# Optimization experiments

Hardware: AMD Instinct MI355X
Metric: run time of the kernel (lower is better)

Reference implementation:

```python
import jax, jax.numpy as jnp
import numpy as np
from jax import lax

SIGMA = 4
TOPK = 9
GRID = 28          # patch grid hardcoded in AnomalyMapGenerator
IMG = 224          # input_size
SCALE = IMG // GRID  # nearest-neighbor upsample factor = 8
KSIZE = 2 * int(4.0 * SIGMA + 0.5) + 1  # 33, as in compute_anomaly_map


def _gaussian_kernel1d():
    x = jnp.arange(KSIZE, dtype=jnp.float32) - KSIZE // 2
    g = jnp.exp(-(x * x) / (2.0 * SIGMA * SIGMA))
    return g / jnp.sum(g)


def _gaussian_blur2d(x):
    # x: [B,1,H,W]; separable gaussian with reflect padding (kornia default)
    g = _gaussian_kernel1d()
    pad = KSIZE // 2
    # blur along H
    xh = jnp.pad(x, ((0, 0), (0, 0), (pad, pad), (0, 0)), mode='reflect')
    xh = lax.conv_general_dilated(xh, g.reshape(1, 1, KSIZE, 1), (1, 1), 'VALID')
    # blur along W
    xw = jnp.pad(xh, ((0, 0), (0, 0), (0, 0), (pad, pad)), mode='reflect')
    return lax.conv_general_dilated(xw, g.reshape(1, 1, 1, KSIZE), (1, 1), 'VALID')


def setup_inputs() -> dict:
    key = jax.random.key(0)
    k1, k2 = jax.random.split(key)
    embedding = jax.random.normal(k1, (3136, 1536), dtype=jnp.float32)
    memory_bank = jax.random.normal(k2, (20000, 1536), dtype=jnp.float32)  # M x D
    return {"embedding": embedding, "memory_bank": memory_bank}


def reference(embedding, memory_bank):
    x2 = jnp.sum(embedding * embedding, axis=-1, keepdims=True)        # [N,1]
    y2 = jnp.sum(memory_bank * memory_bank, axis=-1)                   # [M]
    d2 = x2 + y2[None, :] - 2.0 * (embedding @ memory_bank.T)          # [N,M]
    dist = jnp.sqrt(jnp.maximum(d2, 0.0))
    # topk smallest, ascending (matches torch.topk largest=False)
    neg_top, _ = lax.top_k(-dist, TOPK)
    patch_scores = -neg_top                                            # [N,9]

    # --- compute_anomaly_map ---
    batch = patch_scores.shape[0] // (GRID * GRID)
    amap = patch_scores[:, 0].reshape(batch, 1, GRID, GRID)
    # F.interpolate default mode='nearest' with integer factor 8 == repeat
    amap = jnp.repeat(jnp.repeat(amap, SCALE, axis=2), SCALE, axis=3)  # [B,1,224,224]
    amap = _gaussian_blur2d(amap)

    # --- compute_anomaly_score ---
    idx = jnp.argmax(patch_scores[:, 0])
    confidence = patch_scores[idx]                                     # [9]
    e = jnp.exp(confidence)
    weights = 1.0 - jnp.max(e) / jnp.sum(e)
    score = weights * jnp.max(patch_scores[:, 0])
    return amap, score
```

## Files before the change

kernel.cpp:

```cpp
#include <hip/hip_runtime.h>

typedef __attribute__((ext_vector_type(4))) int i32x4;

#define N_ROWS 3136
#define M_COLS 20000
#define KDIM   1536
#define NCT    157
#define NRT    25
#define PPR    (NCT*9)

#define QSCL   (4.0f / 127.0f)
#define QINV   (127.0f / 4.0f)
#define TWO_S2 (2.0f * QSCL * QSCL)

#define GLOAD_LDS16(g, l) __builtin_amdgcn_global_load_lds( \
    (const __attribute__((address_space(1))) unsigned int*)(g), \
    (__attribute__((address_space(3))) unsigned int*)(l), 16, 0, 0)

__device__ inline void t9_insert(float (&t)[9], float v) {
    #pragma unroll
    for (int s = 8; s >= 1; --s)
        t[s] = __builtin_amdgcn_fmed3f(v, t[s-1], t[s]);
    t[0] = fminf(t[0], v);
}

__device__ inline int q8(float x) {
    int q = (int)rintf(x * QINV);
    q = q > 127 ? 127 : q;
    q = q < -127 ? -127 : q;
    return q & 255;
}

__global__ void cvt_norm_kernel(const float* __restrict__ src,
                                unsigned char* __restrict__ dst,
                                float* __restrict__ norms, int rows) {
    int lane = threadIdx.x & 63;
    int row = blockIdx.x * (blockDim.x >> 6) + (threadIdx.x >> 6);
    if (row >= rows) return;
    const float4* p = (const float4*)(src + (size_t)row * KDIM);
    int* q = (int*)(dst + (size_t)row * KDIM);
    float s = 0.f;
    #pragma unroll
    for (int i = 0; i < 6; ++i) {
        float4 v = p[lane + i * 64];
        s += v.x*v.x + v.y*v.y + v.z*v.z + v.w*v.w;
        q[lane + i * 64] = q8(v.x) | (q8(v.y) << 8) | (q8(v.z) << 16) | (q8(v.w) << 24);
    }
    #pragma unroll
    for (int off = 32; off > 0; off >>= 1) s += __shfl_down(s, off);
    if (lane == 0) norms[row] = s;
}

union SMem {
    unsigned char stg[2][16384];
    struct { float Ds[64 * 129]; float T9[3 * 64 * 9]; } epi;
};

#define STAGE(BUF, KT) do { \
    const int koff_ = (KT) * 64; \
    GLOAD_LDS16(pa[0] + koff_, sm.stg[BUF] + ldsoff[0]); \
    GLOAD_LDS16(pa[1] + koff_, sm.stg[BUF] + ldsoff[1]); \
    GLOAD_LDS16(pb[0] + koff_, sm.stg[BUF] + 8192 + ldsoff[0]); \
    GLOAD_LDS16(pb[1] + koff_, sm.stg[BUF] + 8192 + ldsoff[1]); \
} while (0)

#define KSTEP(CB, NB, KT, PF) do { \
    if (PF) STAGE(NB, (KT) + 1); \
    i32x4 af[4], bfr[4]; \
    _Pragma("unroll") \
    for (int mi = 0; mi < 4; ++mi) \
        af[mi] = *(const i32x4*)(sm.stg[CB] + (wr + mi * 16 + l15) * 64 + kbs); \
    _Pragma("unroll") \
    for (int ni = 0; ni < 4; ++ni) \
        bfr[ni] = *(const i32x4*)(sm.stg[CB] + 8192 + (wc + ni * 16 + l15) * 64 + kbs); \
    _Pragma("unroll") \
    for (int mi = 0; mi < 4; ++mi) \
        _Pragma("unroll") \
        for (int ni = 0; ni < 4; ++ni) \
            acc[mi][ni] = __builtin_amdgcn_mfma_i32_16x16x64_i8(af[mi], bfr[ni], acc[mi][ni], 0, 0, 0); \
    asm volatile("s_waitcnt vmcnt(0)" ::: "memory"); \
    __builtin_amdgcn_s_barrier(); \
} while (0)

__global__ __launch_bounds__(256, 4) void dist_topk_kernel(
    const unsigned char* __restrict__ Aq,
    const unsigned char* __restrict__ Bq,
    const float* __restrict__ x2, const float* __restrict__ y2,
    float* __restrict__ partials)
{
    __shared__ __align__(16) SMem sm;

    const int tid = threadIdx.x;
    const int ct = blockIdx.x, rt = blockIdx.y;
    const int rowBase = rt * 128, colBase = ct * 128;
    const int wave = tid >> 6, lane = tid & 63;

    const unsigned char* pa[2];
    const unsigned char* pb[2];
    int ldsoff[2];
    #pragma unroll
    for (int i = 0; i < 2; ++i) {
        int flat = i * 256 + tid;
        int r = flat >> 2;
        int kk = (((flat & 3) ^ ((flat >> 3) & 3))) * 16;
        int ar = rowBase + r; ar = ar < N_ROWS ? ar : N_ROWS - 1;
        int bc = colBase + r; bc = bc < M_COLS ? bc : M_COLS - 1;
        pa[i] = Aq + (size_t)ar * KDIM + kk;
        pb[i] = Bq + (size_t)bc * KDIM + kk;
        ldsoff[i] = flat * 16;
    }

    const int l15 = lane & 15;
    const int kb = (lane >> 4) * 16;
    const int kbs = kb ^ (((l15 >> 1) & 3) << 4);
    const int g4 = (lane >> 4) * 4;
    const int wr = (wave >> 1) * 64;
    const int wc = (wave & 1) * 64;

    i32x4 acc[4][4] = {};

    STAGE(0, 0);
    asm volatile("s_waitcnt vmcnt(0)" ::: "memory");
    __builtin_amdgcn_s_barrier();

    #pragma unroll 1
    for (int kt = 0; kt < 24; kt += 2) {
        KSTEP(0, 1, kt, 1);
        KSTEP(1, 0, kt + 1, (kt + 2) < 24);
    }

    int ncols = M_COLS - colBase; ncols = ncols < 128 ? ncols : 128;

    #pragma unroll
    for (int pass = 0; pass < 2; ++pass) {
        if ((wave >> 1) == pass) {
            #pragma unroll
            for (int ni = 0; ni < 4; ++ni) {
                int c = wc + ni * 16 + l15;
                int gc = colBase + c;
                float yv = y2[gc < M_COLS ? gc : M_COLS - 1];
                #pragma unroll
                for (int mi = 0; mi < 4; ++mi) {
                    #pragma unroll
                    for (int j = 0; j < 4; ++j) {
                        int rloc = mi * 16 + g4 + j;
                        int gr = rowBase + pass * 64 + rloc;
                        float xv = x2[gr < N_ROWS ? gr : N_ROWS - 1];
                        sm.epi.Ds[rloc * 129 + c] = xv + yv - TWO_S2 * (float)acc[mi][ni][j];
                    }
                }
            }
        }
        __syncthreads();
        int r = tid & 63, q = tid >> 6;
        int grow = rowBase + pass * 64 + r;
        float t9[9];
        #pragma unroll
        for (int s = 0; s < 9; ++s) t9[s] = 3.4e38f;
        int cs = q * 32;
        int ce = (cs + 32 < ncols) ? cs + 32 : ncols;
        for (int c = cs; c < ce; ++c) t9_insert(t9, sm.epi.Ds[r * 129 + c]);
        if (q > 0) {
            #pragma unroll
            for (int s = 0; s < 9; ++s) sm.epi.T9[((q - 1) * 64 + r) * 9 + s] = t9[s];
        }
        __syncthreads();
        if (q == 0 && grow < N_ROWS) {
            #pragma unroll
            for (int qq = 0; qq < 3; ++qq)
                #pragma unroll
                for (int s = 0; s < 9; ++s)
                    t9_insert(t9, sm.epi.T9[(qq * 64 + r) * 9 + s]);
            float* dst = partials + (size_t)grow * PPR + ct * 9;
            #pragma unroll
            for (int s = 0; s < 9; ++s) dst[s] = t9[s];
        }
        __syncthreads();
    }
}

__global__ void merge_topk_kernel(const float* __restrict__ partials,
                                  float* __restrict__ scores) {
    int lane = threadIdx.x & 63;
    int row = blockIdx.x * 4 + (threadIdx.x >> 6);
    const float* p = partials + (size_t)row * PPR;
    float t9[9];
    #pragma unroll
    for (int s = 0; s < 9; ++s) t9[s] = 3.4e38f;
    for (int i = lane; i < PPR; i += 64) {
        float v = p[i];
        if (v < t9[8]) t9_insert(t9, v);
    }
    #pragma unroll
    for (int off = 32; off > 0; off >>= 1) {
        float o[9];
        #pragma unroll
        for (int s = 0; s < 9; ++s) o[s] = __shfl_xor(t9[s], off);
        #pragma unroll
        for (int s = 0; s < 9; ++s)
            if (o[s] < t9[8]) t9_insert(t9, o[s]);
    }
    if (lane == 0) {
        #pragma unroll
        for (int s = 0; s < 9; ++s)
            scores[row * 9 + s] = sqrtf(fmaxf(t9[s], 0.f));
    }
}

__global__ void blur_h_kernel(const float* __restrict__ scores, float* __restrict__ tH) {
    int idx = blockIdx.x * blockDim.x + threadIdx.x;
    if (idx >= 4 * 224 * 28) return;
    int pw = idx % 28, y = (idx / 28) % 224, b = idx / (28 * 224);
    float acc = 0.f, gsum = 0.f;
    #pragma unroll
    for (int k = 0; k < 33; ++k) {
        float xk = (float)(k - 16);
        float w = expf(-xk * xk * (1.0f / 32.0f));
        gsum += w;
        int yy = y - 16 + k;
        yy = yy < 0 ? -yy : yy;
        yy = yy > 223 ? 446 - yy : yy;
        acc += w * scores[(size_t)(b * 784 + (yy >> 3) * 28 + pw) * 9];
    }
    tH[idx] = acc / gsum;
}

__global__ void blur_w_kernel(const float* __restrict__ tH, float* __restrict__ out) {
    int idx = blockIdx.x * blockDim.x + threadIdx.x;
    if (idx >= 4 * 224 * 224) return;
    int x = idx % 224, y = (idx / 224) % 224, b = idx / (224 * 224);
    float acc = 0.f, gsum = 0.f;
    #pragma unroll
    for (int k = 0; k < 33; ++k) {
        float xk = (float)(k - 16);
        float w = expf(-xk * xk * (1.0f / 32.0f));
        gsum += w;
        int xx = x - 16 + k;
        xx = xx < 0 ? -xx : xx;
        xx = xx > 223 ? 446 - xx : xx;
        acc += w * tH[(b * 224 + y) * 28 + (xx >> 3)];
    }
    out[idx] = acc / gsum;
}

__global__ void score_kernel(const float* __restrict__ scores, float* __restrict__ out) {
    __shared__ float vmax[256];
    __shared__ int   vidx[256];
    int tid = threadIdx.x;
    float best = -3.4e38f; int bi = 0x7fffffff;
    for (int r = tid; r < N_ROWS; r += 256) {
        float v = scores[r * 9];
        if (v > best) { best = v; bi = r; }
    }
    vmax[tid] = best; vidx[tid] = bi;
    __syncthreads();
    for (int s = 128; s > 0; s >>= 1) {
        if (tid < s) {
            if (vmax[tid + s] > vmax[tid] ||
                (vmax[tid + s] == vmax[tid] && vidx[tid + s] < vidx[tid])) {
                vmax[tid] = vmax[tid + s]; vidx[tid] = vidx[tid + s];
            }
        }
        __syncthreads();
    }
    if (tid == 0) {
        int idx = vidx[0];
        float es = 0.f, em = -3.4e38f;
        #pragma unroll
        for (int s = 0; s < 9; ++s) {
            float e = expf(scores[idx * 9 + s]);
            es += e; em = fmaxf(em, e);
        }
        out[4 * 224 * 224] = (1.0f - em / es) * vmax[0];
    }
}

extern "C" void kernel_launch(void* const* d_in, const int* in_sizes, int n_in,
                              void* d_out, int out_size, void* d_ws, size_t ws_size,
                              hipStream_t stream) {
    const float* emb = (const float*)d_in[0];
    const float* mb  = (const float*)d_in[1];
    float* out = (float*)d_out;
    char* ws = (char*)d_ws;

    unsigned char* mbq      = (unsigned char*)(ws);
    unsigned char* embq     = (unsigned char*)(ws + 30720000);
    float*         x2       = (float*)(ws + 35536896);
    float*         y2       = (float*)(ws + 35549440);
    float*         partials = (float*)(ws + 35629440);
    float*         scores   = (float*)(ws + 53354112);
    float*         tH       = (float*)(ws + 53467008);

    cvt_norm_kernel<<<M_COLS / 4, 256, 0, stream>>>(mb, mbq, y2, M_COLS);
    cvt_norm_kernel<<<N_ROWS / 4, 256, 0, stream>>>(emb, embq, x2, N_ROWS);
    dist_topk_kernel<<<dim3(NCT, NRT), 256, 0, stream>>>(embq, mbq, x2, y2, partials);
    merge_topk_kernel<<<N_ROWS / 4, 256, 0, stream>>>(partials, scores);
    blur_h_kernel<<<(4 * 224 * 28 + 255) / 256, 256, 0, stream>>>(scores, tH);
    blur_w_kernel<<<(4 * 224 * 224 + 255) / 256, 256, 0, stream>>>(tH, out);
    score_kernel<<<1, 256, 0, stream>>>(scores, out);
}
```

Baseline: 245.1 us.

## Remap workgroups per XCD and shrink epilogue LDS for higher occupancy

Launches the distance/top-k kernel as a 1D grid and remaps block IDs so consecutive tiles on each XCD share column tiles (ct-major order), which is meant to improve L2 reuse of memory-bank tiles. It also splits the epilogue into four 32-row passes using all 8 thread groups with a tree reduction, shrinking the Ds scratch and raising the launch-bounds occupancy hint from 4 to 5. The cost is more barriers and passes in the epilogue, and possibly more register pressure under the tighter bound.

```diff
diff --git a/kernel.cpp b/kernel.cpp
--- a/kernel.cpp
+++ b/kernel.cpp
@@ -7,6 +7,7 @@
 #define KDIM   1536
 #define NCT    157
 #define NRT    25
+#define NWG    (NCT * NRT)
 #define PPR    (NCT*9)
 
 #define QSCL   (4.0f / 127.0f)
@@ -53,7 +54,7 @@
 
 union SMem {
     unsigned char stg[2][16384];
-    struct { float Ds[64 * 129]; float T9[3 * 64 * 9]; } epi;
+    struct { float Ds[32 * 129]; float T9[8 * 32 * 9]; } epi;
 };
 
 #define STAGE(BUF, KT) do { \
@@ -82,7 +83,7 @@
     __builtin_amdgcn_s_barrier(); \
 } while (0)
 
-__global__ __launch_bounds__(256, 4) void dist_topk_kernel(
+__global__ __launch_bounds__(256, 5) void dist_topk_kernel(
     const unsigned char* __restrict__ Aq,
     const unsigned char* __restrict__ Bq,
     const float* __restrict__ x2, const float* __restrict__ y2,
@@ -91,9 +92,14 @@
     __shared__ __align__(16) SMem sm;
 
     const int tid = threadIdx.x;
-    const int ct = blockIdx.x, rt = blockIdx.y;
+    const int wave = tid >> 6, lane = tid & 63;
+
+    int orig = blockIdx.x;
+    int xcd = orig & 7, li = orig >> 3;
+    const int qc = NWG / 8, rc = NWG % 8;
+    int wg = (xcd < rc ? xcd * (qc + 1) : rc * (qc + 1) + (xcd - rc) * qc) + li;
+    const int ct = wg / NRT, rt = wg % NRT;
     const int rowBase = rt * 128, colBase = ct * 128;
-    const int wave = tid >> 6, lane = tid & 63;
 
     const unsigned char* pa[2];
     const unsigned char* pb[2];
@@ -132,50 +138,57 @@
     int ncols = M_COLS - colBase; ncols = ncols < 128 ? ncols : 128;
 
     #pragma unroll
-    for (int pass = 0; pass < 2; ++pass) {
-        if ((wave >> 1) == pass) {
+    for (int p = 0; p < 4; ++p) {
+        __syncthreads();
+        if ((wave >> 1) == (p >> 1)) {
+            const int mi0 = (p & 1) * 2;
             #pragma unroll
             for (int ni = 0; ni < 4; ++ni) {
                 int c = wc + ni * 16 + l15;
                 int gc = colBase + c;
                 float yv = y2[gc < M_COLS ? gc : M_COLS - 1];
                 #pragma unroll
-                for (int mi = 0; mi < 4; ++mi) {
+                for (int mh = 0; mh < 2; ++mh) {
                     #pragma unroll
                     for (int j = 0; j < 4; ++j) {
-                        int rloc = mi * 16 + g4 + j;
-                        int gr = rowBase + pass * 64 + rloc;
+                        int rloc = mh * 16 + g4 + j;
+                        int gr = rowBase + p * 32 + rloc;
                         float xv = x2[gr < N_ROWS ? gr : N_ROWS - 1];
-                        sm.epi.Ds[rloc * 129 + c] = xv + yv - TWO_S2 * (float)acc[mi][ni][j];
+                        sm.epi.Ds[rloc * 129 + c] = xv + yv - TWO_S2 * (float)acc[mi0 + mh][ni][j];
                     }
                 }
             }
         }
         __syncthreads();
-        int r = tid & 63, q = tid >> 6;
-        int grow = rowBase + pass * 64 + r;
+        int r = tid & 31, q8g = tid >> 5;
+        int grow = rowBase + p * 32 + r;
         float t9[9];
         #pragma unroll
         for (int s = 0; s < 9; ++s) t9[s] = 3.4e38f;
-        int cs = q * 32;
-        int ce = (cs + 32 < ncols) ? cs + 32 : ncols;
+        int cs = q8g * 16;
+        int ce = (cs + 16 < ncols) ? cs + 16 : ncols;
         for (int c = cs; c < ce; ++c) t9_insert(t9, sm.epi.Ds[r * 129 + c]);
-        if (q > 0) {
-            #pragma unroll
-            for (int s = 0; s < 9; ++s) sm.epi.T9[((q - 1) * 64 + r) * 9 + s] = t9[s];
-        }
-        __syncthreads();
-        if (q == 0 && grow < N_ROWS) {
-            #pragma unroll
-            for (int qq = 0; qq < 3; ++qq)
+        #pragma unroll
+        for (int s = 0; s < 9; ++s) sm.epi.T9[(q8g * 32 + r) * 9 + s] = t9[s];
+        __syncthreads();
+        if (q8g < 4) {
+            #pragma unroll
+            for (int s = 0; s < 9; ++s)
+                t9_insert(t9, sm.epi.T9[((q8g + 4) * 32 + r) * 9 + s]);
+            #pragma unroll
+            for (int s = 0; s < 9; ++s) sm.epi.T9[(q8g * 32 + r) * 9 + s] = t9[s];
+        }
+        __syncthreads();
+        if (q8g == 0 && grow < N_ROWS) {
+            #pragma unroll
+            for (int qq = 1; qq < 4; ++qq)
                 #pragma unroll
                 for (int s = 0; s < 9; ++s)
-                    t9_insert(t9, sm.epi.T9[(qq * 64 + r) * 9 + s]);
+                    t9_insert(t9, sm.epi.T9[(qq * 32 + r) * 9 + s]);
             float* dst = partials + (size_t)grow * PPR + ct * 9;
             #pragma unroll
             for (int s = 0; s < 9; ++s) dst[s] = t9[s];
         }
-        __syncthreads();
     }
 }
 
@@ -293,7 +306,7 @@
 
     cvt_norm_kernel<<<M_COLS / 4, 256, 0, stream>>>(mb, mbq, y2, M_COLS);
     cvt_norm_kernel<<<N_ROWS / 4, 256, 0, stream>>>(emb, embq, x2, N_ROWS);
-    dist_topk_kernel<<<dim3(NCT, NRT), 256, 0, stream>>>(embq, mbq, x2, y2, partials);
+    dist_topk_kernel<<<NWG, 256, 0, stream>>>(embq, mbq, x2, y2, partials);
     merge_topk_kernel<<<N_ROWS / 4, 256, 0, stream>>>(partials, scores);
     blur_h_kernel<<<(4 * 224 * 28 + 255) / 256, 256, 0, stream>>>(scores, tH);
     blur_w_kernel<<<(4 * 224 * 224 + 255) / 256, 256, 0, stream>>>(tH, out);
```

After: 353.0 us. 44.0% more time.
